# Kernel tuning notes

Measured on AMD Instinct MI355X. Metric: run time of the kernel, lower is better.

## Reference

```python
import jax, jax.numpy as jnp
import numpy as np

HEADS = 12
EMBED = 768
HEAD_DIM = EMBED // HEADS


def setup_inputs() -> dict:
    key = jax.random.key(0)
    kx, kw, kb = jax.random.split(key, 3)
    x = jax.random.normal(kx, (8, 1024, EMBED), dtype=jnp.float32)
    # nn.Linear(embed, 3*embed): weight (3E, E), bias (3E,)
    W_qkv = jax.random.normal(kw, (3 * EMBED, EMBED), dtype=jnp.float32) * (1.0 / np.sqrt(EMBED))
    b_qkv = jax.random.normal(kb, (3 * EMBED,), dtype=jnp.float32) * 0.01
    return {"x": x, "W_qkv": W_qkv, "b_qkv": b_qkv}


def reference(x, W_qkv, b_qkv):
    b, n, e = x.shape
    qkv = x @ W_qkv.T + b_qkv                       # (b, n, 3E)
    qkv = qkv.reshape(b, n, HEADS, 3 * HEAD_DIM)    # (b, n, h, 3d)
    q, k, v = jnp.split(qkv, 3, axis=-1)            # each (b, n, h, d)
    scores = jnp.einsum('bihd,bjhd->bijh', q, k) / np.sqrt(HEAD_DIM)
    attn = jax.nn.softmax(scores, axis=-2)          # softmax over keys j (dim=-2)
    out = jnp.einsum('bijh,bjhd->bihd', attn, v)
    return out.reshape(b, n, e)
```

## Files before the change

kernel.cpp:

```cpp
#include <hip/hip_runtime.h>
#include <hip/hip_bf16.h>
#include <cstdint>

#define BATCH 8
#define SEQ   1024
#define EMB   768
#define HEADS 12
#define HDIM  64
#define C3    2304
#define MROWS (BATCH*SEQ)

typedef __attribute__((ext_vector_type(8)))  short bf16x8;
typedef __attribute__((ext_vector_type(4)))  short bf16x4;
typedef __attribute__((ext_vector_type(4)))  float f32x4;
typedef __attribute__((ext_vector_type(16))) float f32x16;

static __device__ inline short f2bf(float f) {
    union { float f; uint32_t u; } v; v.f = f;
    uint32_t u = v.u + 0x7fff + ((v.u >> 16) & 1);
    return (short)(u >> 16);
}

static __device__ inline void gload_lds16(const short* g, short* l) {
    __builtin_amdgcn_global_load_lds(
        (const __attribute__((address_space(1))) void*)g,
        (__attribute__((address_space(3))) void*)l, 16, 0, 0);
}

__global__ __launch_bounds__(256) void f32_to_bf16(const float* __restrict__ in,
                                                   short* __restrict__ out, int n8) {
    int i = blockIdx.x * 256 + threadIdx.x;
    if (i >= n8) return;
    float4 v0 = ((const float4*)in)[i * 2];
    float4 v1 = ((const float4*)in)[i * 2 + 1];
    bf16x8 o = { f2bf(v0.x), f2bf(v0.y), f2bf(v0.z), f2bf(v0.w),
                 f2bf(v1.x), f2bf(v1.y), f2bf(v1.z), f2bf(v1.w) };
    ((bf16x8*)out)[i] = o;
}

#define CHK 528

__global__ __launch_bounds__(256) void qkv_gemm_mfma(const short* __restrict__ xb,
                                                     const short* __restrict__ Wb,
                                                     const float* __restrict__ bias,
                                                     short* __restrict__ qkvb) {
    __shared__ short As[2][8 * CHK];
    __shared__ short Bs[2][8 * CHK];

    const int bx = blockIdx.x;
    const int by = blockIdx.y;
    const int t = threadIdx.x;
    const int w = t >> 6;
    const int lane = t & 63;
    const int m0 = by * 128, n0 = bx * 128;
    const int wm = (w & 1) * 64, wn = (w >> 1) * 64;

    const int srow = lane >> 2;
    const int scol = (lane & 3) * 8;
    const short* ga0 = xb + (size_t)(m0 + w * 16 + srow) * EMB + scol;
    const short* ga1 = xb + (size_t)(m0 + 64 + w * 16 + srow) * EMB + scol;
    const short* gb0 = Wb + (size_t)(n0 + w * 16 + srow) * EMB + scol;
    const short* gb1 = Wb + (size_t)(n0 + 64 + w * 16 + srow) * EMB + scol;

    const int l5  = lane >> 5;
    const int r31 = lane & 31;
    const int rlo = lane & 15;
    const int rhi = (lane >> 4) & 1;
    int aoff[2], boff[2];
    #pragma unroll
    for (int mt = 0; mt < 2; ++mt)
        aoff[mt] = ((wm >> 4) + 2 * mt + rhi) * CHK + rlo * 32 + l5 * 8;
    #pragma unroll
    for (int nt = 0; nt < 2; ++nt)
        boff[nt] = ((wn >> 4) + 2 * nt + rhi) * CHK + rlo * 32 + l5 * 8;

    f32x16 acc[2][2] = {};

    gload_lds16(ga0, &As[0][w * CHK]);
    gload_lds16(ga1, &As[0][(4 + w) * CHK]);
    gload_lds16(gb0, &Bs[0][w * CHK]);
    gload_lds16(gb1, &Bs[0][(4 + w) * CHK]);
    __syncthreads();

    for (int kt = 0; kt < 24; ++kt) {
        const int cur = kt & 1, nxt = cur ^ 1;
        if (kt < 23) {
            const int ko = (kt + 1) * 32;
            gload_lds16(ga0 + ko, &As[nxt][w * CHK]);
            gload_lds16(ga1 + ko, &As[nxt][(4 + w) * CHK]);
            gload_lds16(gb0 + ko, &Bs[nxt][w * CHK]);
            gload_lds16(gb1 + ko, &Bs[nxt][(4 + w) * CHK]);
        }
        bf16x8 a[2][2], b[2][2];
        #pragma unroll
        for (int mt = 0; mt < 2; ++mt)
            #pragma unroll
            for (int s = 0; s < 2; ++s)
                a[mt][s] = *(bf16x8*)&As[cur][aoff[mt] + s * 16];
        #pragma unroll
        for (int nt = 0; nt < 2; ++nt)
            #pragma unroll
            for (int s = 0; s < 2; ++s)
                b[nt][s] = *(bf16x8*)&Bs[cur][boff[nt] + s * 16];
        #pragma unroll
        for (int mt = 0; mt < 2; ++mt)
            #pragma unroll
            for (int nt = 0; nt < 2; ++nt)
                #pragma unroll
                for (int s = 0; s < 2; ++s)
                    acc[mt][nt] = __builtin_amdgcn_mfma_f32_32x32x16_bf16(
                        a[mt][s], b[nt][s], acc[mt][nt], 0, 0, 0);
        __syncthreads();
    }

    float bsv[2], scl[2];
    #pragma unroll
    for (int nt = 0; nt < 2; ++nt) {
        int n = n0 + wn + nt * 32 + r31;
        bsv[nt] = bias[n];
        scl[nt] = ((n % 192) < 64) ? 0.125f : 1.0f;
    }
    #pragma unroll
    for (int mt = 0; mt < 2; ++mt)
        #pragma unroll
        for (int nt = 0; nt < 2; ++nt) {
            int n = n0 + wn + nt * 32 + r31;
            #pragma unroll
            for (int reg = 0; reg < 16; ++reg) {
                int row = (reg & 3) + 8 * (reg >> 2) + 4 * l5;
                int m = m0 + wm + mt * 32 + row;
                float v = (acc[mt][nt][reg] + bsv[nt]) * scl[nt];
                qkvb[(size_t)m * C3 + n] = f2bf(v);
            }
        }
}

__global__ __launch_bounds__(256) void v_transpose(const short* __restrict__ qkvb,
                                                   short* __restrict__ vt) {
    __shared__ int Lt[64][65];

    const int bh = blockIdx.x;
    const int jt = blockIdx.y;
    const int b = bh / HEADS, h = bh % HEADS;
    const int t = threadIdx.x;
    const int j0 = jt * 64;
    const size_t base = (size_t)b * SEQ * C3 + (size_t)h * 192 + 128;

    #pragma unroll
    for (int p = 0; p < 2; ++p) {
        int idx = p * 256 + t;
        int j = idx >> 3, d0 = (idx & 7) * 8;
        bf16x8 v = *(const bf16x8*)(qkvb + base + (size_t)(j0 + j) * C3 + d0);
        #pragma unroll
        for (int u = 0; u < 8; ++u)
            Lt[d0 + u][j] = (int)(unsigned short)v[u];
    }
    __syncthreads();
    #pragma unroll
    for (int p = 0; p < 2; ++p) {
        int idx = p * 256 + t;
        int d = idx >> 3, c8 = (idx & 7) * 8;
        bf16x8 o;
        #pragma unroll
        for (int u = 0; u < 8; ++u)
            o[u] = (short)Lt[d][c8 + u];
        *(bf16x8*)(vt + ((size_t)bh * 64 + d) * SEQ + j0 + c8) = o;
    }
}

#define LDP 72

__global__ __launch_bounds__(256, 4) void attn_mfma(const short* __restrict__ qkvb,
                                                    const short* __restrict__ vt,
                                                    float* __restrict__ out) {
    __shared__ short Ks[64][LDP];
    __shared__ short Vt[64][LDP];
    __shared__ short Ps[64][LDP];

    const int bx   = blockIdx.x;
    const int qt   = bx & 15;
    const int h    = (bx >> 4) % HEADS;
    const int b    = bx / (16 * HEADS);
    const int t    = threadIdx.x;
    const int w    = t >> 6;
    const int lane = t & 63;
    const int c    = lane & 15;
    const int q    = lane >> 4;
    const int i0   = qt * 64;

    const size_t base = (size_t)b * SEQ * C3 + (size_t)h * 192;
    const short* vtb = vt + (size_t)(b * HEADS + h) * 64 * SEQ;

    #pragma unroll
    for (int p = 0; p < 2; ++p) {
        int idx = p * 256 + t;
        int i = idx >> 3, d0 = (idx & 7) << 3;
        *(bf16x8*)&Ps[i][d0] =
            *(const bf16x8*)(qkvb + base + (size_t)(i0 + i) * C3 + d0);
    }
    __syncthreads();
    const bf16x8 aq0 = *(bf16x8*)&Ps[w * 16 + c][q * 8];
    const bf16x8 aq1 = *(bf16x8*)&Ps[w * 16 + c][32 + q * 8];

    f32x4 o[4] = {{0.f,0.f,0.f,0.f},{0.f,0.f,0.f,0.f},
                  {0.f,0.f,0.f,0.f},{0.f,0.f,0.f,0.f}};
    float l_acc = 0.f;

    for (int kt = 0; kt < 16; ++kt) {
        const int j0 = kt * 64;
        __syncthreads();
        #pragma unroll
        for (int p = 0; p < 2; ++p) {
            int idx = p * 256 + t;
            int j = idx >> 3, d0 = (idx & 7) << 3;
            *(bf16x8*)&Ks[j][d0] =
                *(const bf16x8*)(qkvb + base + 64 + (size_t)(j0 + j) * C3 + d0);
        }
        #pragma unroll
        for (int p = 0; p < 2; ++p) {
            int idx = p * 256 + t;
            int d = idx >> 3, j8 = (idx & 7) << 3;
            *(bf16x8*)&Vt[d][j8] =
                *(const bf16x8*)(vtb + (size_t)d * SEQ + j0 + j8);
        }
        __syncthreads();

        f32x4 s[4];
        #pragma unroll
        for (int mt = 0; mt < 4; ++mt) {
            bf16x8 a0 = *(bf16x8*)&Ks[mt * 16 + c][q * 8];
            bf16x8 a1 = *(bf16x8*)&Ks[mt * 16 + c][32 + q * 8];
            f32x4 acc = {0.f, 0.f, 0.f, 0.f};
            acc = __builtin_amdgcn_mfma_f32_16x16x32_bf16(a0, aq0, acc, 0, 0, 0);
            acc = __builtin_amdgcn_mfma_f32_16x16x32_bf16(a1, aq1, acc, 0, 0, 0);
            s[mt] = acc;
        }

        #pragma unroll
        for (int mt = 0; mt < 4; ++mt) {
            float p0 = __expf(s[mt][0]);
            float p1 = __expf(s[mt][1]);
            float p2 = __expf(s[mt][2]);
            float p3 = __expf(s[mt][3]);
            l_acc += (p0 + p1) + (p2 + p3);
            bf16x4 pw = { f2bf(p0), f2bf(p1), f2bf(p2), f2bf(p3) };
            *(bf16x4*)&Ps[w * 16 + c][mt * 16 + 4 * q] = pw;
        }

        bf16x8 ap0 = *(bf16x8*)&Ps[w * 16 + c][q * 8];
        bf16x8 ap1 = *(bf16x8*)&Ps[w * 16 + c][32 + q * 8];
        #pragma unroll
        for (int dt = 0; dt < 4; ++dt) {
            bf16x8 b0 = *(bf16x8*)&Vt[dt * 16 + c][q * 8];
            bf16x8 b1 = *(bf16x8*)&Vt[dt * 16 + c][32 + q * 8];
            o[dt] = __builtin_amdgcn_mfma_f32_16x16x32_bf16(ap0, b0, o[dt], 0, 0, 0);
            o[dt] = __builtin_amdgcn_mfma_f32_16x16x32_bf16(ap1, b1, o[dt], 0, 0, 0);
        }
    }

    l_acc += __shfl_xor(l_acc, 16, 64);
    l_acc += __shfl_xor(l_acc, 32, 64);
    float linv[4];
    #pragma unroll
    for (int r = 0; r < 4; ++r)
        linv[r] = 1.0f / __shfl(l_acc, 4 * q + r, 64);

    #pragma unroll
    for (int dt = 0; dt < 4; ++dt)
        #pragma unroll
        for (int r = 0; r < 4; ++r) {
            int i = w * 16 + q * 4 + r;
            out[((size_t)b * SEQ + i0 + i) * EMB + h * HDIM + dt * 16 + c]
                = o[dt][r] * linv[r];
        }
}

extern "C" void kernel_launch(void* const* d_in, const int* in_sizes, int n_in,
                              void* d_out, int out_size, void* d_ws, size_t ws_size,
                              hipStream_t stream) {
    const float* x    = (const float*)d_in[0];
    const float* W    = (const float*)d_in[1];
    const float* bias = (const float*)d_in[2];
    float* out = (float*)d_out;

    short* xb   = (short*)d_ws;
    short* Wb   = xb + (size_t)MROWS * EMB;
    short* qkvb = Wb + (size_t)C3 * EMB;
    short* vt   = qkvb + (size_t)MROWS * C3;

    f32_to_bf16<<<(MROWS * EMB / 8 + 255) / 256, 256, 0, stream>>>(x, xb, MROWS * EMB / 8);
    f32_to_bf16<<<(C3 * EMB / 8 + 255) / 256, 256, 0, stream>>>(W, Wb, C3 * EMB / 8);

    dim3 g1(C3 / 128, MROWS / 128);
    qkv_gemm_mfma<<<g1, 256, 0, stream>>>(xb, Wb, bias, qkvb);

    dim3 g2(BATCH * HEADS, SEQ / 64);
    v_transpose<<<g2, 256, 0, stream>>>(qkvb, vt);

    attn_mfma<<<BATCH * HEADS * (SEQ / 64), 256, 0, stream>>>(qkvb, vt, out);
}
```

Before: 183.8 us.

## Pack GEMM operands into MFMA fragment layout and load directly from global

The fp32-to-bf16 conversion kernels now write x and W in a tiled layout matching the 32x32x16 MFMA operand fragments, 32 rows by 16 k per 512-element slice. The QKV GEMM drops its LDS double buffer and barriers and has each wave load its fragments straight from global memory with contiguous 16-byte loads. This removes LDS traffic and synchronisation. In exchange each wave fetches its own A and B fragments with no sharing inside the block, which relies on L2/L1 for reuse and exposes global latency, since the only prefetch is the compiler scheduling of the unrolled loop.

```diff
diff --git a/kernel.cpp b/kernel.cpp
--- a/kernel.cpp
+++ b/kernel.cpp
@@ -9,6 +9,7 @@
 #define HDIM  64
 #define C3    2304
 #define MROWS (BATCH*SEQ)
+#define KSLC  (EMB / 16)
 
 typedef __attribute__((ext_vector_type(8)))  short bf16x8;
 typedef __attribute__((ext_vector_type(4)))  short bf16x4;
@@ -21,96 +22,60 @@
     return (short)(u >> 16);
 }
 
-static __device__ inline void gload_lds16(const short* g, short* l) {
-    __builtin_amdgcn_global_load_lds(
-        (const __attribute__((address_space(1))) void*)g,
-        (__attribute__((address_space(3))) void*)l, 16, 0, 0);
-}
-
-__global__ __launch_bounds__(256) void f32_to_bf16(const float* __restrict__ in,
-                                                   short* __restrict__ out, int n8) {
-    int i = blockIdx.x * 256 + threadIdx.x;
-    if (i >= n8) return;
-    float4 v0 = ((const float4*)in)[i * 2];
-    float4 v1 = ((const float4*)in)[i * 2 + 1];
-    bf16x8 o = { f2bf(v0.x), f2bf(v0.y), f2bf(v0.z), f2bf(v0.w),
-                 f2bf(v1.x), f2bf(v1.y), f2bf(v1.z), f2bf(v1.w) };
-    ((bf16x8*)out)[i] = o;
-}
-
-#define CHK 528
-
-__global__ __launch_bounds__(256) void qkv_gemm_mfma(const short* __restrict__ xb,
-                                                     const short* __restrict__ Wb,
+__global__ __launch_bounds__(256) void pack_bf16(const float* __restrict__ in,
+                                                 short* __restrict__ out) {
+    const int tid = blockIdx.x * 256 + threadIdx.x;
+    const int r    = tid & 31;
+    const int ks   = (tid >> 5) % KSLC;
+    const int tile = tid / (KSLC * 32);
+    const int row  = tile * 32 + r;
+
+    const float* src = in + (size_t)row * EMB + ks * 16;
+    float4 v0 = ((const float4*)src)[0];
+    float4 v1 = ((const float4*)src)[1];
+    float4 v2 = ((const float4*)src)[2];
+    float4 v3 = ((const float4*)src)[3];
+    bf16x8 o0 = { f2bf(v0.x), f2bf(v0.y), f2bf(v0.z), f2bf(v0.w),
+                  f2bf(v1.x), f2bf(v1.y), f2bf(v1.z), f2bf(v1.w) };
+    bf16x8 o1 = { f2bf(v2.x), f2bf(v2.y), f2bf(v2.z), f2bf(v2.w),
+                  f2bf(v3.x), f2bf(v3.y), f2bf(v3.z), f2bf(v3.w) };
+    short* dst = out + (size_t)tid * 16;
+    *(bf16x8*)(dst)     = o0;
+    *(bf16x8*)(dst + 8) = o1;
+}
+
+__global__ __launch_bounds__(256) void qkv_gemm_mfma(const short* __restrict__ xb2,
+                                                     const short* __restrict__ Wb2,
                                                      const float* __restrict__ bias,
                                                      short* __restrict__ qkvb) {
-    __shared__ short As[2][8 * CHK];
-    __shared__ short Bs[2][8 * CHK];
-
     const int bx = blockIdx.x;
     const int by = blockIdx.y;
     const int t = threadIdx.x;
     const int w = t >> 6;
     const int lane = t & 63;
+    const int l5  = lane >> 5;
+    const int r31 = lane & 31;
     const int m0 = by * 128, n0 = bx * 128;
     const int wm = (w & 1) * 64, wn = (w >> 1) * 64;
 
-    const int srow = lane >> 2;
-    const int scol = (lane & 3) * 8;
-    const short* ga0 = xb + (size_t)(m0 + w * 16 + srow) * EMB + scol;
-    const short* ga1 = xb + (size_t)(m0 + 64 + w * 16 + srow) * EMB + scol;
-    const short* gb0 = Wb + (size_t)(n0 + w * 16 + srow) * EMB + scol;
-    const short* gb1 = Wb + (size_t)(n0 + 64 + w * 16 + srow) * EMB + scol;
-
-    const int l5  = lane >> 5;
-    const int r31 = lane & 31;
-    const int rlo = lane & 15;
-    const int rhi = (lane >> 4) & 1;
-    int aoff[2], boff[2];
-    #pragma unroll
-    for (int mt = 0; mt < 2; ++mt)
-        aoff[mt] = ((wm >> 4) + 2 * mt + rhi) * CHK + rlo * 32 + l5 * 8;
-    #pragma unroll
-    for (int nt = 0; nt < 2; ++nt)
-        boff[nt] = ((wn >> 4) + 2 * nt + rhi) * CHK + rlo * 32 + l5 * 8;
+    const int laneoff = r31 * 16 + l5 * 8;
+    const short* pa0 = xb2 + ((size_t)((m0 + wm) >> 5) * KSLC) * 512 + laneoff;
+    const short* pa1 = pa0 + (size_t)KSLC * 512;
+    const short* pb0 = Wb2 + ((size_t)((n0 + wn) >> 5) * KSLC) * 512 + laneoff;
+    const short* pb1 = pb0 + (size_t)KSLC * 512;
 
     f32x16 acc[2][2] = {};
 
-    gload_lds16(ga0, &As[0][w * CHK]);
-    gload_lds16(ga1, &As[0][(4 + w) * CHK]);
-    gload_lds16(gb0, &Bs[0][w * CHK]);
-    gload_lds16(gb1, &Bs[0][(4 + w) * CHK]);
-    __syncthreads();
-
-    for (int kt = 0; kt < 24; ++kt) {
-        const int cur = kt & 1, nxt = cur ^ 1;
-        if (kt < 23) {
-            const int ko = (kt + 1) * 32;
-            gload_lds16(ga0 + ko, &As[nxt][w * CHK]);
-            gload_lds16(ga1 + ko, &As[nxt][(4 + w) * CHK]);
-            gload_lds16(gb0 + ko, &Bs[nxt][w * CHK]);
-            gload_lds16(gb1 + ko, &Bs[nxt][(4 + w) * CHK]);
-        }
-        bf16x8 a[2][2], b[2][2];
-        #pragma unroll
-        for (int mt = 0; mt < 2; ++mt)
-            #pragma unroll
-            for (int s = 0; s < 2; ++s)
-                a[mt][s] = *(bf16x8*)&As[cur][aoff[mt] + s * 16];
-        #pragma unroll
-        for (int nt = 0; nt < 2; ++nt)
-            #pragma unroll
-            for (int s = 0; s < 2; ++s)
-                b[nt][s] = *(bf16x8*)&Bs[cur][boff[nt] + s * 16];
-        #pragma unroll
-        for (int mt = 0; mt < 2; ++mt)
-            #pragma unroll
-            for (int nt = 0; nt < 2; ++nt)
-                #pragma unroll
-                for (int s = 0; s < 2; ++s)
-                    acc[mt][nt] = __builtin_amdgcn_mfma_f32_32x32x16_bf16(
-                        a[mt][s], b[nt][s], acc[mt][nt], 0, 0, 0);
-        __syncthreads();
+    #pragma unroll 4
+    for (int ks = 0; ks < KSLC; ++ks) {
+        bf16x8 a0 = *(const bf16x8*)(pa0 + ks * 512);
+        bf16x8 a1 = *(const bf16x8*)(pa1 + ks * 512);
+        bf16x8 b0 = *(const bf16x8*)(pb0 + ks * 512);
+        bf16x8 b1 = *(const bf16x8*)(pb1 + ks * 512);
+        acc[0][0] = __builtin_amdgcn_mfma_f32_32x32x16_bf16(a0, b0, acc[0][0], 0, 0, 0);
+        acc[0][1] = __builtin_amdgcn_mfma_f32_32x32x16_bf16(a0, b1, acc[0][1], 0, 0, 0);
+        acc[1][0] = __builtin_amdgcn_mfma_f32_32x32x16_bf16(a1, b0, acc[1][0], 0, 0, 0);
+        acc[1][1] = __builtin_amdgcn_mfma_f32_32x32x16_bf16(a1, b1, acc[1][1], 0, 0, 0);
     }
 
     float bsv[2], scl[2];
@@ -283,16 +248,16 @@
     const float* bias = (const float*)d_in[2];
     float* out = (float*)d_out;
 
-    short* xb   = (short*)d_ws;
-    short* Wb   = xb + (size_t)MROWS * EMB;
-    short* qkvb = Wb + (size_t)C3 * EMB;
+    short* xb2  = (short*)d_ws;
+    short* Wb2  = xb2 + (size_t)MROWS * EMB;
+    short* qkvb = Wb2 + (size_t)C3 * EMB;
     short* vt   = qkvb + (size_t)MROWS * C3;
 
-    f32_to_bf16<<<(MROWS * EMB / 8 + 255) / 256, 256, 0, stream>>>(x, xb, MROWS * EMB / 8);
-    f32_to_bf16<<<(C3 * EMB / 8 + 255) / 256, 256, 0, stream>>>(W, Wb, C3 * EMB / 8);
+    pack_bf16<<<MROWS * KSLC / 256, 256, 0, stream>>>(x, xb2);
+    pack_bf16<<<C3 * KSLC / 256, 256, 0, stream>>>(W, Wb2);
 
     dim3 g1(C3 / 128, MROWS / 128);
-    qkv_gemm_mfma<<<g1, 256, 0, stream>>>(xb, Wb, bias, qkvb);
+    qkv_gemm_mfma<<<g1, 256, 0, stream>>>(xb2, Wb2, bias, qkvb);
 
     dim3 g2(BATCH * HEADS, SEQ / 64);
     v_transpose<<<g2, 256, 0, stream>>>(qkvb, vt);
```

Measured after the change: 181.9 us. No clear change (-1.0%).
